# Kernel tuning notes

Measured on AMD Instinct MI355X. Metric: run time of the kernel, lower is better.

Reference implementation:

```python
import jax, jax.numpy as jnp
import numpy as np

DIM = 384
HEADS = 6
HEAD_DIM = DIM // HEADS
HIDDEN = 4 * DIM
K_NEIGH = 8
EPS = 1e-5


def layer_norm(x, w, b):
    mu = jnp.mean(x, axis=-1, keepdims=True)
    var = jnp.mean(jnp.square(x - mu), axis=-1, keepdims=True)
    return (x - mu) * jax.lax.rsqrt(var + EPS) * w + b


def setup_inputs() -> dict:
    key = jax.random.key(0)
    ks = jax.random.split(key, 16)
    B, N, D = 8, 2048, DIM
    s = 0.02
    inp = {
        "x": jax.random.normal(ks[0], (B, N, D), dtype=jnp.float32),
        "knn_index": jax.random.randint(ks[1], (B * K_NEIGH * N,), 0, B * N, dtype=jnp.int64),
        "norm1_w": jnp.ones((D,), jnp.float32),
        "norm1_b": jnp.zeros((D,), jnp.float32),
        "qkv_w": jax.random.normal(ks[2], (D, 3 * D), jnp.float32) * s,
        "proj_w": jax.random.normal(ks[3], (D, D), jnp.float32) * s,
        "proj_b": jnp.zeros((D,), jnp.float32),
        "knn_w": jax.random.normal(ks[4], (2 * D, D), jnp.float32) * s,
        "knn_b": jnp.zeros((D,), jnp.float32),
        "merge_w": jax.random.normal(ks[5], (2 * D, D), jnp.float32) * s,
        "merge_b": jnp.zeros((D,), jnp.float32),
        "norm2_w": jnp.ones((D,), jnp.float32),
        "norm2_b": jnp.zeros((D,), jnp.float32),
        "fc1_w": jax.random.normal(ks[6], (D, HIDDEN), jnp.float32) * s,
        "fc1_b": jnp.zeros((HIDDEN,), jnp.float32),
        "fc2_w": jax.random.normal(ks[7], (HIDDEN, D), jnp.float32) * s,
        "fc2_b": jnp.zeros((D,), jnp.float32),
    }
    return inp


def _forward(x, knn_index, norm1_w, norm1_b, qkv_w, proj_w, proj_b,
             knn_w, knn_b, merge_w, merge_b, norm2_w, norm2_b,
             fc1_w, fc1_b, fc2_w, fc2_b):
    B, N, D = x.shape
    norm_x = layer_norm(x, norm1_w, norm1_b)

    # --- multi-head self-attention (no qkv bias, no dropout) ---
    qkv = (norm_x @ qkv_w).reshape(B, N, 3, HEADS, HEAD_DIM)
    q, k, v = qkv[:, :, 0], qkv[:, :, 1], qkv[:, :, 2]  # [B,N,H,Dh]
    scale = HEAD_DIM ** -0.5
    attn = jnp.einsum("bnhd,bmhd->bhnm", q, k) * scale
    attn = jax.nn.softmax(attn, axis=-1)
    x_1 = jnp.einsum("bhnm,bmhd->bnhd", attn, v).reshape(B, N, D)
    x_1 = x_1 @ proj_w + proj_b

    # --- graph feature: gather k=8 neighbors, diff-concat ---
    feat = norm_x.reshape(B * N, D)[knn_index].reshape(B, K_NEIGH, N, D)
    xq = norm_x[:, None]  # [B,1,N,D]
    knn_f = jnp.concatenate([feat - xq, jnp.broadcast_to(xq, feat.shape)], axis=-1)
    knn_f = jax.nn.leaky_relu(knn_f @ knn_w + knn_b, negative_slope=0.2)
    knn_f = jnp.max(knn_f, axis=1)  # max-pool over neighbors -> [B,N,D]

    x_1 = jnp.concatenate([x_1, knn_f], axis=-1) @ merge_w + merge_b
    x = x + x_1

    # --- MLP block ---
    h = layer_norm(x, norm2_w, norm2_b)
    h = jax.nn.gelu(h @ fc1_w + fc1_b, approximate=False)
    x = x + (h @ fc2_w + fc2_b)
    return x


def reference(x, knn_index, norm1_w, norm1_b, qkv_w, proj_w, proj_b,
              knn_w, knn_b, merge_w, merge_b, norm2_w, norm2_b,
              fc1_w, fc1_b, fc2_w, fc2_b):
    return _forward(x, knn_index, norm1_w, norm1_b, qkv_w, proj_w, proj_b,
                    knn_w, knn_b, merge_w, merge_b, norm2_w, norm2_b,
                    fc1_w, fc1_b, fc2_w, fc2_b)
```

## Files before the change

kernel.cpp:

```cpp
#include <hip/hip_runtime.h>

typedef unsigned short u16;
typedef unsigned int u32;
typedef __attribute__((ext_vector_type(8))) short short8;
typedef __attribute__((ext_vector_type(4))) u16 u16x4;
typedef __attribute__((ext_vector_type(2))) u32 u32x2;
typedef __attribute__((ext_vector_type(4))) float f32x4;

__device__ __forceinline__ u16 f2bf(float f) {
  unsigned u = __float_as_uint(f);
  u += 0x7fffu + ((u >> 16) & 1u);
  return (u16)(u >> 16);
}
__device__ __forceinline__ float b2f(u16 v) { return __uint_as_float((u32)v << 16); }

#define GLD16(g, l)                                                        \
  __builtin_amdgcn_global_load_lds(                                        \
      (const __attribute__((address_space(1))) void*)(g),                  \
      (__attribute__((address_space(3))) void*)(l), 16, 0, 0)

struct TJobs {
  const float* in[7];
  unsigned long long outoff[7];
  int ld[7], row0[7], K[7], blkend[7];
};
__global__ void transpose_all_kernel(TJobs J, char* __restrict__ ws) {
  int bx = blockIdx.x;
  int ji = 0;
  while (bx >= J.blkend[ji]) ji++;
  int base = (ji == 0) ? 0 : J.blkend[ji - 1];
  int i = (bx - base) * 256 + threadIdx.x;
  int K = J.K[ji];
  int j = i / K, k = i - j * K;
  u16* out = (u16*)(ws + J.outoff[ji]);
  out[(size_t)j * K + k] = f2bf(J.in[ji][(size_t)(J.row0[ji] + k) * J.ld[ji] + j]);
}

__global__ void ln_kernel(const float* __restrict__ in, const float* __restrict__ w,
                          const float* __restrict__ b, u16* __restrict__ out) {
  int row = blockIdx.x, t = threadIdx.x;
  const float* r = in + (size_t)row * 384;
  float v[6];
  float s = 0.f;
#pragma unroll
  for (int i = 0; i < 6; i++) { v[i] = r[t + 64 * i]; s += v[i]; }
#pragma unroll
  for (int off = 32; off > 0; off >>= 1) s += __shfl_xor(s, off);
  float mu = s * (1.f / 384.f);
  float q = 0.f;
#pragma unroll
  for (int i = 0; i < 6; i++) { float d = v[i] - mu; q += d * d; }
#pragma unroll
  for (int off = 32; off > 0; off >>= 1) q += __shfl_xor(q, off);
  float rstd = rsqrtf(q * (1.f / 384.f) + 1e-5f);
#pragma unroll
  for (int i = 0; i < 6; i++) {
    int j = t + 64 * i;
    out[(size_t)row * 384 + j] = f2bf((v[i] - mu) * rstd * w[j] + b[j]);
  }
}

template <int MODE, int TN>
__global__ __launch_bounds__(256) void gemm_kernel(
    const u16* __restrict__ A, const u16* __restrict__ Bt,
    int M, int N, int K, int ldc,
    const float* __restrict__ bias, const float* __restrict__ res,
    void* __restrict__ out0, void* __restrict__ out1, void* __restrict__ out2,
    void* __restrict__ out3) {
  __shared__ u16 Als[2][128 * 32];
  __shared__ u16 Bls[2][TN * 32];
  const int NJ = TN / 32;
  const int MB = M >> 7;
  int mb = blockIdx.x % MB, nb = blockIdx.x / MB;
  int m0 = mb << 7, n0 = nb * TN;
  int tid = threadIdx.x;
  int lane = tid & 63, w = tid >> 6;
  int wm = (w >> 1) << 6, wn = (w & 1) * (TN / 2);
  int l15 = lane & 15, l16 = lane >> 4;
  const f32x4 fz = {0.f, 0.f, 0.f, 0.f};
  f32x4 acc[4][NJ];
#pragma unroll
  for (int i = 0; i < 4; i++)
#pragma unroll
    for (int j = 0; j < NJ; j++) acc[i][j] = fz;

  const int strow = lane >> 2, stch = (lane & 3) * 8;
  const u16* Ag = A + (size_t)(m0 + w * 32 + strow) * K + stch;
  const u16* Bg = Bt + (size_t)(n0 + w * (TN / 4) + strow) * K + stch;
  u16* Al0 = &Als[0][(w * 32) * 32];
  u16* Al1 = &Als[1][(w * 32) * 32];
  u16* Bl0 = &Bls[0][(w * (TN / 4)) * 32];
  u16* Bl1 = &Bls[1][(w * (TN / 4)) * 32];

  for (int k0 = 0; k0 < K; k0 += 64) {
    __syncthreads();
    GLD16(Ag + k0, Al0);
    GLD16(Ag + k0 + (size_t)16 * K, Al0 + 16 * 32);
    GLD16(Ag + k0 + 32, Al1);
    GLD16(Ag + k0 + 32 + (size_t)16 * K, Al1 + 16 * 32);
    GLD16(Bg + k0, Bl0);
    GLD16(Bg + k0 + 32, Bl1);
    if (TN == 128) {
      GLD16(Bg + k0 + (size_t)16 * K, Bl0 + 16 * 32);
      GLD16(Bg + k0 + 32 + (size_t)16 * K, Bl1 + 16 * 32);
    }
    asm volatile("s_waitcnt vmcnt(0)" ::: "memory");
    __syncthreads();
#pragma unroll
    for (int kk = 0; kk < 2; kk++) {
      short8 af[4], bfr[NJ];
#pragma unroll
      for (int i = 0; i < 4; i++)
        af[i] = *(const short8*)&Als[kk][(wm + i * 16 + l15) * 32 + l16 * 8];
#pragma unroll
      for (int j = 0; j < NJ; j++)
        bfr[j] = *(const short8*)&Bls[kk][(wn + j * 16 + l15) * 32 + l16 * 8];
      __builtin_amdgcn_s_setprio(1);
#pragma unroll
      for (int i = 0; i < 4; i++)
#pragma unroll
        for (int j = 0; j < NJ; j++)
          acc[i][j] = __builtin_amdgcn_mfma_f32_16x16x32_bf16(af[i], bfr[j], acc[i][j], 0, 0, 0);
      __builtin_amdgcn_s_setprio(0);
    }
  }

#pragma unroll
  for (int i = 0; i < 4; i++)
#pragma unroll
    for (int j = 0; j < NJ; j++)
#pragma unroll
      for (int r = 0; r < 4; r++) {
        int row = m0 + wm + i * 16 + l16 * 4 + r;
        int col = n0 + wn + j * 16 + l15;
        float v = acc[i][j][r];
        if (MODE == 1) {
          ((u16*)out0)[(size_t)row * ldc + col] = f2bf(v + bias[col]);
        } else if (MODE == 2) {
          if (col < 384) {
            ((u16*)out0)[(size_t)row * 384 + col] = f2bf(v * 0.18033688011112042f);
          } else if (col < 768) {
            ((u16*)out1)[(size_t)row * 384 + col - 384] = f2bf(v);
          } else if (col < 1152) {
            int df = col - 768, hh = df >> 6, dd = df & 63;
            ((u16*)out2)[(((size_t)(row >> 11) * 6 + hh) * 64 + dd) * 2048 + (row & 2047)] = f2bf(v);
          } else {
            ((u16*)out3)[(size_t)row * 768 + (col - 1152)] = f2bf(v);
          }
        } else if (MODE == 3) {
          ((float*)out0)[(size_t)row * ldc + col] = v + bias[col] + res[(size_t)row * ldc + col];
        } else if (MODE == 4) {
          float u = v + bias[col];
          float g = 0.5f * u * (1.f + erff(u * 0.70710678118f));
          ((u16*)out0)[(size_t)row * ldc + col] = f2bf(g);
        }
      }
}

#define ASTR 80
__global__ __launch_bounds__(256) void attn_kernel(const u16* __restrict__ qb,
                                                   const u16* __restrict__ kb,
                                                   const u16* __restrict__ vtb,
                                                   u16* __restrict__ ab) {
  __shared__ u16 Kls[64 * ASTR];
  __shared__ u16 Vls[64 * ASTR];
  __shared__ u16 Pls[64 * ASTR];
  int bx = blockIdx.x;
  int q0 = (bx & 31) << 6;
  int h = (bx >> 5) % 6;
  int b = bx / 192;
  int tid = threadIdx.x, lane = tid & 63, w = tid >> 6;
  int l15 = lane & 15, l16 = lane >> 4;

  const size_t qbase = (size_t)(b * 2048 + q0) * 384 + h * 64;
  {
    int idx0 = tid, idx1 = 256 + tid;
    *(short8*)&Kls[(idx0 >> 3) * ASTR + (idx0 & 7) * 8] =
        *(const short8*)&qb[qbase + (size_t)(idx0 >> 3) * 384 + (idx0 & 7) * 8];
    *(short8*)&Kls[(idx1 >> 3) * ASTR + (idx1 & 7) * 8] =
        *(const short8*)&qb[qbase + (size_t)(idx1 >> 3) * 384 + (idx1 & 7) * 8];
  }
  __syncthreads();
  short8 aq0 = *(const short8*)&Kls[(w * 16 + l15) * ASTR + l16 * 8];
  short8 aq1 = *(const short8*)&Kls[(w * 16 + l15) * ASTR + 32 + l16 * 8];

  const f32x4 fz = {0.f, 0.f, 0.f, 0.f};
  f32x4 ot[4];
#pragma unroll
  for (int di = 0; di < 4; di++) ot[di] = fz;
  float m = -1e30f, lpart = 0.f;

  const size_t kbase = (size_t)b * 2048 * 384 + h * 64;
  const size_t vbase = ((size_t)b * 6 + h) * 64 * 2048;
  const int srow = tid >> 3, sch = (tid & 7) * 8;

  short8 kr0 = *(const short8*)&kb[kbase + (size_t)srow * 384 + sch];
  short8 kr1 = *(const short8*)&kb[kbase + (size_t)(srow + 32) * 384 + sch];
  short8 vr0 = *(const short8*)&vtb[vbase + (size_t)srow * 2048 + sch];
  short8 vr1 = *(const short8*)&vtb[vbase + (size_t)(srow + 32) * 2048 + sch];

  for (int t = 0; t < 32; t++) {
    __syncthreads();
    *(short8*)&Kls[srow * ASTR + sch] = kr0;
    *(short8*)&Kls[(srow + 32) * ASTR + sch] = kr1;
    *(short8*)&Vls[srow * ASTR + sch] = vr0;
    *(short8*)&Vls[(srow + 32) * ASTR + sch] = vr1;
    if (t + 1 < 32) {
      int j0n = (t + 1) << 6;
      kr0 = *(const short8*)&kb[kbase + (size_t)(j0n + srow) * 384 + sch];
      kr1 = *(const short8*)&kb[kbase + (size_t)(j0n + srow + 32) * 384 + sch];
      vr0 = *(const short8*)&vtb[vbase + (size_t)srow * 2048 + j0n + sch];
      vr1 = *(const short8*)&vtb[vbase + (size_t)(srow + 32) * 2048 + j0n + sch];
    }
    __syncthreads();

    f32x4 s[4];
    __builtin_amdgcn_s_setprio(1);
#pragma unroll
    for (int nj = 0; nj < 4; nj++) {
      short8 kf0 = *(const short8*)&Kls[(nj * 16 + l15) * ASTR + l16 * 8];
      short8 kf1 = *(const short8*)&Kls[(nj * 16 + l15) * ASTR + 32 + l16 * 8];
      s[nj] = __builtin_amdgcn_mfma_f32_16x16x32_bf16(kf0, aq0, fz, 0, 0, 0);
      s[nj] = __builtin_amdgcn_mfma_f32_16x16x32_bf16(kf1, aq1, s[nj], 0, 0, 0);
    }
    __builtin_amdgcn_s_setprio(0);

    float mloc = fmaxf(fmaxf(s[0][0], s[0][1]), s[0][2]);
    mloc = fmaxf(fmaxf(mloc, s[0][3]), s[1][0]);
    mloc = fmaxf(fmaxf(mloc, s[1][1]), s[1][2]);
    mloc = fmaxf(fmaxf(mloc, s[1][3]), s[2][0]);
    mloc = fmaxf(fmaxf(mloc, s[2][1]), s[2][2]);
    mloc = fmaxf(fmaxf(mloc, s[2][3]), s[3][0]);
    mloc = fmaxf(fmaxf(mloc, s[3][1]), s[3][2]);
    mloc = fmaxf(mloc, s[3][3]);
    if (__any(mloc > m)) {
      float mt = fmaxf(mloc, __shfl_xor(mloc, 16));
      mt = fmaxf(mt, __shfl_xor(mt, 32));
      float mn = fmaxf(m, mt);
      float alpha = exp2f(m - mn);
      m = mn;
      lpart *= alpha;
#pragma unroll
      for (int di = 0; di < 4; di++)
#pragma unroll
        for (int r = 0; r < 4; r++) ot[di][r] *= alpha;
    }

#pragma unroll
    for (int nj = 0; nj < 4; nj++) {
      float p0 = exp2f(s[nj][0] - m);
      float p1 = exp2f(s[nj][1] - m);
      float p2 = exp2f(s[nj][2] - m);
      float p3 = exp2f(s[nj][3] - m);
      lpart += (p0 + p1) + (p2 + p3);
      u32 lo = (__float_as_uint(p1) & 0xffff0000u) | (__float_as_uint(p0) >> 16);
      u32 hi = (__float_as_uint(p3) & 0xffff0000u) | (__float_as_uint(p2) >> 16);
      u32x2 pr = {lo, hi};
      *(u32x2*)&Pls[(w * 16 + l15) * ASTR + nj * 16 + l16 * 4] = pr;
    }

    __builtin_amdgcn_s_setprio(1);
#pragma unroll
    for (int ks = 0; ks < 2; ks++) {
      short8 pb = *(const short8*)&Pls[(w * 16 + l15) * ASTR + ks * 32 + l16 * 8];
#pragma unroll
      for (int di = 0; di < 4; di++) {
        short8 vf = *(const short8*)&Vls[(di * 16 + l15) * ASTR + ks * 32 + l16 * 8];
        ot[di] = __builtin_amdgcn_mfma_f32_16x16x32_bf16(vf, pb, ot[di], 0, 0, 0);
      }
    }
    __builtin_amdgcn_s_setprio(0);
  }

  lpart += __shfl_xor(lpart, 16);
  lpart += __shfl_xor(lpart, 32);
  float inv = 1.f / lpart;
  int token = b * 2048 + q0 + w * 16 + l15;
#pragma unroll
  for (int di = 0; di < 4; di++) {
    u16x4 pk4 = {f2bf(ot[di][0] * inv), f2bf(ot[di][1] * inv),
                 f2bf(ot[di][2] * inv), f2bf(ot[di][3] * inv)};
    *(u16x4*)&ab[(size_t)token * 384 + h * 64 + di * 16 + l16 * 4] = pk4;
  }
}

__global__ void knn_kernel(const u16* __restrict__ GH, const int* __restrict__ kidx,
                           const float* __restrict__ kbias, u16* __restrict__ cat) {
  int f = blockIdx.x * 256 + threadIdx.x;
  if (f >= 16384 * 96) return;
  int token = f / 96, j4 = f - token * 96;
  int b = token >> 11, n = token & 2047;
  int j = j4 * 4;
  u16x4 gs = *(const u16x4*)&GH[(size_t)token * 768 + j];
  u16x4 hs = *(const u16x4*)&GH[(size_t)token * 768 + 384 + j];
  float4 kb4 = *(const float4*)&kbias[j];
  float dx = b2f(hs[0]) - b2f(gs[0]) + kb4.x;
  float dy = b2f(hs[1]) - b2f(gs[1]) + kb4.y;
  float dz = b2f(hs[2]) - b2f(gs[2]) + kb4.z;
  float dw = b2f(hs[3]) - b2f(gs[3]) + kb4.w;
  float mx = -1e30f, my = -1e30f, mz = -1e30f, mw = -1e30f;
#pragma unroll
  for (int k = 0; k < 8; k++) {
    int t = kidx[(b * 8 + k) * 2048 + n];
    u16x4 g = *(const u16x4*)&GH[(size_t)t * 768 + j];
    mx = fmaxf(mx, b2f(g[0]) + dx);
    my = fmaxf(my, b2f(g[1]) + dy);
    mz = fmaxf(mz, b2f(g[2]) + dz);
    mw = fmaxf(mw, b2f(g[3]) + dw);
  }
  mx = mx > 0.f ? mx : 0.2f * mx;
  my = my > 0.f ? my : 0.2f * my;
  mz = mz > 0.f ? mz : 0.2f * mz;
  mw = mw > 0.f ? mw : 0.2f * mw;
  u16x4 pk = {f2bf(mx), f2bf(my), f2bf(mz), f2bf(mw)};
  *(u16x4*)&cat[(size_t)token * 768 + 384 + j] = pk;
}

extern "C" void kernel_launch(void* const* d_in, const int* in_sizes, int n_in,
                              void* d_out, int out_size, void* d_ws, size_t ws_size,
                              hipStream_t stream) {
  const float* x       = (const float*)d_in[0];
  const int*   kidx    = (const int*)d_in[1];
  const float* n1w     = (const float*)d_in[2];
  const float* n1b     = (const float*)d_in[3];
  const float* qkv_w   = (const float*)d_in[4];
  const float* proj_w  = (const float*)d_in[5];
  const float* proj_b  = (const float*)d_in[6];
  const float* knn_w   = (const float*)d_in[7];
  const float* knn_b   = (const float*)d_in[8];
  const float* merge_w = (const float*)d_in[9];
  const float* merge_b = (const float*)d_in[10];
  const float* n2w     = (const float*)d_in[11];
  const float* n2b     = (const float*)d_in[12];
  const float* fc1_w   = (const float*)d_in[13];
  const float* fc1_b   = (const float*)d_in[14];
  const float* fc2_w   = (const float*)d_in[15];
  const float* fc2_b   = (const float*)d_in[16];
  float* out = (float*)d_out;
  char* ws = (char*)d_ws;

  u16* wbig   = (u16*)(ws + 0);
  u16* wproj  = (u16*)(ws + 1474560);
  u16* wmerge = (u16*)(ws + 1769472);
  u16* wfc1   = (u16*)(ws + 2359296);
  u16* wfc2   = (u16*)(ws + 3538944);
  u16* nx     = (u16*)(ws + 4718592);
  u16* qbf    = (u16*)(ws + 17301504);
  u16* kbf    = (u16*)(ws + 29884416);
  u16* vtb    = (u16*)(ws + 42467328);
  u16* GH     = (u16*)(ws + 55050240);
  float* xmid = (float*)(ws + 105381888);
  u16* cat = kbf;
  u16* n2  = qbf;
  u16* abf = nx;
  u16* hbf = GH;

  TJobs J;
  J.in[0] = qkv_w;   J.outoff[0] = 0;       J.ld[0] = 1152; J.row0[0] = 0;   J.K[0] = 384;  J.blkend[0] = 1728;
  J.in[1] = knn_w;   J.outoff[1] = 884736;  J.ld[1] = 384;  J.row0[1] = 0;   J.K[1] = 384;  J.blkend[1] = 2304;
  J.in[2] = knn_w;   J.outoff[2] = 1179648; J.ld[2] = 384;  J.row0[2] = 384; J.K[2] = 384;  J.blkend[2] = 2880;
  J.in[3] = proj_w;  J.outoff[3] = 1474560; J.ld[3] = 384;  J.row0[3] = 0;   J.K[3] = 384;  J.blkend[3] = 3456;
  J.in[4] = merge_w; J.outoff[4] = 1769472; J.ld[4] = 384;  J.row0[4] = 0;   J.K[4] = 768;  J.blkend[4] = 4608;
  J.in[5] = fc1_w;   J.outoff[5] = 2359296; J.ld[5] = 1536; J.row0[5] = 0;   J.K[5] = 384;  J.blkend[5] = 6912;
  J.in[6] = fc2_w;   J.outoff[6] = 3538944; J.ld[6] = 384;  J.row0[6] = 0;   J.K[6] = 1536; J.blkend[6] = 9216;
  transpose_all_kernel<<<9216, 256, 0, stream>>>(J, ws);

  ln_kernel<<<16384, 64, 0, stream>>>(x, n1w, n1b, nx);
  gemm_kernel<2, 128><<<128 * 15, 256, 0, stream>>>(nx, wbig, 16384, 1920, 384, 0, nullptr, nullptr, qbf, kbf, vtb, GH);
  attn_kernel<<<1536, 256, 0, stream>>>(qbf, kbf, vtb, abf);
  knn_kernel<<<6144, 256, 0, stream>>>(GH, kidx, knn_b, cat);
  gemm_kernel<1, 64><<<128 * 6, 256, 0, stream>>>(abf, wproj, 16384, 384, 384, 768, proj_b, nullptr, cat, nullptr, nullptr, nullptr);
  gemm_kernel<3, 64><<<128 * 6, 256, 0, stream>>>(cat, wmerge, 16384, 384, 768, 384, merge_b, x, xmid, nullptr, nullptr, nullptr);
  ln_kernel<<<16384, 64, 0, stream>>>(xmid, n2w, n2b, n2);
  gemm_kernel<4, 128><<<128 * 12, 256, 0, stream>>>(n2, wfc1, 16384, 1536, 384, 1536, fc1_b, nullptr, hbf, nullptr, nullptr, nullptr);
  gemm_kernel<3, 64><<<128 * 6, 256, 0, stream>>>(hbf, wfc2, 16384, 384, 1536, 384, fc2_b, xmid, out, nullptr, nullptr, nullptr);
}
```

Measured before the change: 306.1 us.

## Fold projection into merge weights and read split A operands directly

Precomputes proj_w @ merge_w[:384] and the combined bias on device, so the attention output feeds the merge GEMM directly and the separate projection GEMM is dropped. The merge GEMM gains a split-A mode that reads its first K half from the attention buffer and its second half from a compact knn buffer, which removes the concatenated intermediate. This adds a small per-call weight-combine kernel and changes where bf16 rounding happens in the projection path.

```diff
diff --git a/kernel.cpp b/kernel.cpp
--- a/kernel.cpp
+++ b/kernel.cpp
@@ -22,7 +22,7 @@
 struct TJobs {
   const float* in[7];
   unsigned long long outoff[7];
-  int ld[7], row0[7], K[7], blkend[7];
+  int ld[7], row0[7], K[7], ostr[7], ocol[7], blkend[7];
 };
 __global__ void transpose_all_kernel(TJobs J, char* __restrict__ ws) {
   int bx = blockIdx.x;
@@ -33,7 +33,35 @@
   int K = J.K[ji];
   int j = i / K, k = i - j * K;
   u16* out = (u16*)(ws + J.outoff[ji]);
-  out[(size_t)j * K + k] = f2bf(J.in[ji][(size_t)(J.row0[ji] + k) * J.ld[ji] + j]);
+  out[(size_t)j * J.ostr[ji] + J.ocol[ji] + k] = f2bf(J.in[ji][(size_t)(J.row0[ji] + k) * J.ld[ji] + j]);
+}
+
+__global__ void wcombine_kernel(const float* __restrict__ Wp, const float* __restrict__ Wm,
+                                u16* __restrict__ outB) {
+  int i = blockIdx.x * 256 + threadIdx.x;
+  int n = i % 384, kq = i / 384;
+  int k = kq * 4;
+  float s0 = 0.f, s1 = 0.f, s2 = 0.f, s3 = 0.f;
+  for (int m = 0; m < 384; m++) {
+    float wm = Wm[(size_t)m * 384 + n];
+    s0 += Wp[(size_t)(k + 0) * 384 + m] * wm;
+    s1 += Wp[(size_t)(k + 1) * 384 + m] * wm;
+    s2 += Wp[(size_t)(k + 2) * 384 + m] * wm;
+    s3 += Wp[(size_t)(k + 3) * 384 + m] * wm;
+  }
+  outB[(size_t)n * 768 + k + 0] = f2bf(s0);
+  outB[(size_t)n * 768 + k + 1] = f2bf(s1);
+  outB[(size_t)n * 768 + k + 2] = f2bf(s2);
+  outB[(size_t)n * 768 + k + 3] = f2bf(s3);
+}
+
+__global__ void wbias_kernel(const float* __restrict__ pb, const float* __restrict__ Wm,
+                             const float* __restrict__ mb, float* __restrict__ outb) {
+  int n = blockIdx.x * 256 + threadIdx.x;
+  if (n >= 384) return;
+  float s = mb[n];
+  for (int m = 0; m < 384; m++) s += pb[m] * Wm[(size_t)m * 384 + n];
+  outb[n] = s;
 }
 
 __global__ void ln_kernel(const float* __restrict__ in, const float* __restrict__ w,
@@ -60,9 +88,9 @@
   }
 }
 
-template <int MODE, int TN>
+template <int MODE, int TN, bool SPLITA>
 __global__ __launch_bounds__(256) void gemm_kernel(
-    const u16* __restrict__ A, const u16* __restrict__ Bt,
+    const u16* __restrict__ A, const u16* __restrict__ A2, const u16* __restrict__ Bt,
     int M, int N, int K, int ldc,
     const float* __restrict__ bias, const float* __restrict__ res,
     void* __restrict__ out0, void* __restrict__ out1, void* __restrict__ out2,
@@ -85,7 +113,8 @@
     for (int j = 0; j < NJ; j++) acc[i][j] = fz;
 
   const int strow = lane >> 2, stch = (lane & 3) * 8;
-  const u16* Ag = A + (size_t)(m0 + w * 32 + strow) * K + stch;
+  const int KA = SPLITA ? 384 : K;
+  const size_t arowoff = (size_t)(m0 + w * 32 + strow) * KA + stch;
   const u16* Bg = Bt + (size_t)(n0 + w * (TN / 4) + strow) * K + stch;
   u16* Al0 = &Als[0][(w * 32) * 32];
   u16* Al1 = &Als[1][(w * 32) * 32];
@@ -93,11 +122,16 @@
   u16* Bl1 = &Bls[1][(w * (TN / 4)) * 32];
 
   for (int k0 = 0; k0 < K; k0 += 64) {
+    const u16* Asrc;
+    if (SPLITA)
+      Asrc = (k0 < 384) ? (A + arowoff + k0) : (A2 + arowoff + (k0 - 384));
+    else
+      Asrc = A + arowoff + k0;
     __syncthreads();
-    GLD16(Ag + k0, Al0);
-    GLD16(Ag + k0 + (size_t)16 * K, Al0 + 16 * 32);
-    GLD16(Ag + k0 + 32, Al1);
-    GLD16(Ag + k0 + 32 + (size_t)16 * K, Al1 + 16 * 32);
+    GLD16(Asrc, Al0);
+    GLD16(Asrc + (size_t)16 * KA, Al0 + 16 * 32);
+    GLD16(Asrc + 32, Al1);
+    GLD16(Asrc + 32 + (size_t)16 * KA, Al1 + 16 * 32);
     GLD16(Bg + k0, Bl0);
     GLD16(Bg + k0 + 32, Bl1);
     if (TN == 128) {
@@ -285,7 +319,7 @@
 }
 
 __global__ void knn_kernel(const u16* __restrict__ GH, const int* __restrict__ kidx,
-                           const float* __restrict__ kbias, u16* __restrict__ cat) {
+                           const float* __restrict__ kbias, u16* __restrict__ knnb) {
   int f = blockIdx.x * 256 + threadIdx.x;
   if (f >= 16384 * 96) return;
   int token = f / 96, j4 = f - token * 96;
@@ -313,7 +347,7 @@
   mz = mz > 0.f ? mz : 0.2f * mz;
   mw = mw > 0.f ? mw : 0.2f * mw;
   u16x4 pk = {f2bf(mx), f2bf(my), f2bf(mz), f2bf(mw)};
-  *(u16x4*)&cat[(size_t)token * 768 + 384 + j] = pk;
+  *(u16x4*)&knnb[(size_t)token * 384 + j] = pk;
 }
 
 extern "C" void kernel_launch(void* const* d_in, const int* in_sizes, int n_in,
@@ -339,39 +373,40 @@
   float* out = (float*)d_out;
   char* ws = (char*)d_ws;
 
-  u16* wbig   = (u16*)(ws + 0);
-  u16* wproj  = (u16*)(ws + 1474560);
-  u16* wmerge = (u16*)(ws + 1769472);
-  u16* wfc1   = (u16*)(ws + 2359296);
-  u16* wfc2   = (u16*)(ws + 3538944);
-  u16* nx     = (u16*)(ws + 4718592);
-  u16* qbf    = (u16*)(ws + 17301504);
-  u16* kbf    = (u16*)(ws + 29884416);
-  u16* vtb    = (u16*)(ws + 42467328);
-  u16* GH     = (u16*)(ws + 55050240);
-  float* xmid = (float*)(ws + 105381888);
-  u16* cat = kbf;
-  u16* n2  = qbf;
-  u16* abf = nx;
-  u16* hbf = GH;
+  u16* wbig    = (u16*)(ws + 0);
+  float* wmbias= (float*)(ws + 1474560);
+  u16* wmergeB = (u16*)(ws + 1769472);
+  u16* wfc1    = (u16*)(ws + 2359296);
+  u16* wfc2    = (u16*)(ws + 3538944);
+  u16* nx      = (u16*)(ws + 4718592);
+  u16* qbf     = (u16*)(ws + 17301504);
+  u16* kbf     = (u16*)(ws + 29884416);
+  u16* vtb     = (u16*)(ws + 42467328);
+  u16* GH      = (u16*)(ws + 55050240);
+  float* xmid  = (float*)(ws + 105381888);
+  u16* knnb = kbf;
+  u16* n2   = qbf;
+  u16* abf  = nx;
+  u16* hbf  = GH;
 
   TJobs J;
-  J.in[0] = qkv_w;   J.outoff[0] = 0;       J.ld[0] = 1152; J.row0[0] = 0;   J.K[0] = 384;  J.blkend[0] = 1728;
-  J.in[1] = knn_w;   J.outoff[1] = 884736;  J.ld[1] = 384;  J.row0[1] = 0;   J.K[1] = 384;  J.blkend[1] = 2304;
-  J.in[2] = knn_w;   J.outoff[2] = 1179648; J.ld[2] = 384;  J.row0[2] = 384; J.K[2] = 384;  J.blkend[2] = 2880;
-  J.in[3] = proj_w;  J.outoff[3] = 1474560; J.ld[3] = 384;  J.row0[3] = 0;   J.K[3] = 384;  J.blkend[3] = 3456;
-  J.in[4] = merge_w; J.outoff[4] = 1769472; J.ld[4] = 384;  J.row0[4] = 0;   J.K[4] = 768;  J.blkend[4] = 4608;
-  J.in[5] = fc1_w;   J.outoff[5] = 2359296; J.ld[5] = 1536; J.row0[5] = 0;   J.K[5] = 384;  J.blkend[5] = 6912;
-  J.in[6] = fc2_w;   J.outoff[6] = 3538944; J.ld[6] = 384;  J.row0[6] = 0;   J.K[6] = 1536; J.blkend[6] = 9216;
-  transpose_all_kernel<<<9216, 256, 0, stream>>>(J, ws);
+  J.in[0] = qkv_w;   J.outoff[0] = 0;       J.ld[0] = 1152; J.row0[0] = 0;   J.K[0] = 384;  J.ostr[0] = 384;  J.ocol[0] = 0;   J.blkend[0] = 1728;
+  J.in[1] = knn_w;   J.outoff[1] = 884736;  J.ld[1] = 384;  J.row0[1] = 0;   J.K[1] = 384;  J.ostr[1] = 384;  J.ocol[1] = 0;   J.blkend[1] = 2304;
+  J.in[2] = knn_w;   J.outoff[2] = 1179648; J.ld[2] = 384;  J.row0[2] = 384; J.K[2] = 384;  J.ostr[2] = 384;  J.ocol[2] = 0;   J.blkend[2] = 2880;
+  J.in[3] = merge_w; J.outoff[3] = 1769472; J.ld[3] = 384;  J.row0[3] = 384; J.K[3] = 384;  J.ostr[3] = 768;  J.ocol[3] = 384; J.blkend[3] = 3456;
+  J.in[4] = fc1_w;   J.outoff[4] = 2359296; J.ld[4] = 1536; J.row0[4] = 0;   J.K[4] = 384;  J.ostr[4] = 384;  J.ocol[4] = 0;   J.blkend[4] = 5760;
+  J.in[5] = fc2_w;   J.outoff[5] = 3538944; J.ld[5] = 384;  J.row0[5] = 0;   J.K[5] = 1536; J.ostr[5] = 1536; J.ocol[5] = 0;   J.blkend[5] = 8064;
+  J.in[6] = fc2_w;   J.outoff[6] = 0;       J.ld[6] = 1;    J.row0[6] = 0;   J.K[6] = 1;    J.ostr[6] = 1;    J.ocol[6] = 0;   J.blkend[6] = 8064;
+  transpose_all_kernel<<<8064, 256, 0, stream>>>(J, ws);
+  wcombine_kernel<<<144, 256, 0, stream>>>(proj_w, merge_w, wmergeB);
+  wbias_kernel<<<2, 256, 0, stream>>>(proj_b, merge_w, merge_b, wmbias);
 
   ln_kernel<<<16384, 64, 0, stream>>>(x, n1w, n1b, nx);
-  gemm_kernel<2, 128><<<128 * 15, 256, 0, stream>>>(nx, wbig, 16384, 1920, 384, 0, nullptr, nullptr, qbf, kbf, vtb, GH);
+  gemm_kernel<2, 128, false><<<128 * 15, 256, 0, stream>>>(nx, nullptr, wbig, 16384, 1920, 384, 0, nullptr, nullptr, qbf, kbf, vtb, GH);
   attn_kernel<<<1536, 256, 0, stream>>>(qbf, kbf, vtb, abf);
-  knn_kernel<<<6144, 256, 0, stream>>>(GH, kidx, knn_b, cat);
-  gemm_kernel<1, 64><<<128 * 6, 256, 0, stream>>>(abf, wproj, 16384, 384, 384, 768, proj_b, nullptr, cat, nullptr, nullptr, nullptr);
-  gemm_kernel<3, 64><<<128 * 6, 256, 0, stream>>>(cat, wmerge, 16384, 384, 768, 384, merge_b, x, xmid, nullptr, nullptr, nullptr);
+  knn_kernel<<<6144, 256, 0, stream>>>(GH, kidx, knn_b, knnb);
+  gemm_kernel<3, 64, true><<<128 * 6, 256, 0, stream>>>(abf, knnb, wmergeB, 16384, 384, 768, 384, wmbias, x, xmid, nullptr, nullptr, nullptr);
   ln_kernel<<<16384, 64, 0, stream>>>(xmid, n2w, n2b, n2);
-  gemm_kernel<4, 128><<<128 * 12, 256, 0, stream>>>(n2, wfc1, 16384, 1536, 384, 1536, fc1_b, nullptr, hbf, nullptr, nullptr, nullptr);
-  gemm_kernel<3, 64><<<128 * 6, 256, 0, stream>>>(hbf, wfc2, 16384, 384, 1536, 384, fc2_b, xmid, out, nullptr, nullptr, nullptr);
-}
+  gemm_kernel<4, 128, false><<<128 * 12, 256, 0, stream>>>(n2, nullptr, wfc1, 16384, 1536, 384, 1536, fc1_b, nullptr, hbf, nullptr, nullptr, nullptr);
+  gemm_kernel<3, 64, false><<<128 * 6, 256, 0, stream>>>(hbf, nullptr, wfc2, 16384, 384, 1536, 384, fc2_b, xmid, out, nullptr, nullptr, nullptr);
+}
```

After: 343.8 us. 1.12x slower.
